# Kernel tuning notes

Hardware: AMD Instinct MI355X
Metric: run time of the kernel (lower is better)

The kernel has to match this reference:

```python
import jax, jax.numpy as jnp
import numpy as np


def setup_inputs() -> dict:
    B, n, C = 256, 512, 256
    key = jax.random.key(0)
    ks = jax.random.split(key, 8)
    s = 1.0 / np.sqrt(C)
    return {
        "P": jax.random.normal(ks[0], (B, n, C), dtype=jnp.float32),
        "id": jax.random.randint(ks[1], (B,), 0, n, dtype=jnp.int64),
        "Wq": jax.random.normal(ks[2], (C, C), dtype=jnp.float32) * s,
        "bq": jax.random.normal(ks[3], (C,), dtype=jnp.float32) * s,
        "Wk": jax.random.normal(ks[4], (C, C), dtype=jnp.float32) * s,
        "bk": jax.random.normal(ks[5], (C,), dtype=jnp.float32) * s,
        "Wv": jax.random.normal(ks[6], (C, C), dtype=jnp.float32) * s,
        "bv": jax.random.normal(ks[7], (C,), dtype=jnp.float32) * s,
    }


def reference(P, id, Wq, bq, Wk, bk, Wv, bv):
    # Gather the query row per batch first, then project (same math as
    # projecting all rows and gathering, but avoids redundant compute).
    B = P.shape[0]
    p_sel = P[jnp.arange(B), id]                 # [B, C]
    Q = p_sel @ Wq.T + bq                        # [B, C]
    K = jnp.einsum('bnc,dc->bnd', P, Wk) + bk    # [B, n, C]
    V = jnp.einsum('bnc,dc->bnd', P, Wv) + bv    # [B, n, C]
    scores = jnp.einsum('bc,bnc->bn', Q, K)      # [B, n] (no sqrt scaling, per source)
    attn = jax.nn.softmax(scores, axis=-1)       # [B, n]
    out = jnp.einsum('bn,bnc->bc', attn, V)      # [B, C]
    return out
```

## Files before the change

kernel.cpp:

```cpp
#include <hip/hip_runtime.h>

#define BATCH 256
#define NROW  512
#define CDIM  256
#define WAVES 8
#define RPW   (NROW / WAVES)
#define CHK   16
#define NCHK  (RPW / CHK)

__global__ __launch_bounds__(256) void qk_kernel(
    const float* __restrict__ P, const int* __restrict__ idx,
    const float* __restrict__ Wq, const float* __restrict__ bq,
    const float* __restrict__ Wk, float* __restrict__ qk) {
  __shared__ float s_psel[CDIM];
  __shared__ float s_q[CDIM];
  const int b = blockIdx.x;
  const int t = threadIdx.x;

  const float* prow = P + ((size_t)b * NROW + (size_t)idx[b]) * CDIM;
  s_psel[t] = prow[t];
  __syncthreads();

  {
    const float4* wq4 = (const float4*)(Wq + (size_t)t * CDIM);
    const float4* ps4 = (const float4*)s_psel;
    float acc = 0.f;
#pragma unroll 8
    for (int c4 = 0; c4 < CDIM / 4; ++c4) {
      float4 w = wq4[c4], p = ps4[c4];
      acc += w.x * p.x + w.y * p.y + w.z * p.z + w.w * p.w;
    }
    s_q[t] = acc + bq[t];
  }
  __syncthreads();

  {
    float acc = 0.f;
#pragma unroll 8
    for (int d = 0; d < CDIM; ++d) acc += s_q[d] * Wk[(size_t)d * CDIM + t];
    qk[(size_t)b * CDIM + t] = acc;
  }
}

__global__ __launch_bounds__(512) void attn_fused_kernel(
    const float* __restrict__ P, const float* __restrict__ qk,
    const float* __restrict__ Wv, const float* __restrict__ bv,
    float* __restrict__ out) {
  const int b = blockIdx.x;
  const int t = threadIdx.x;
  const int lane = t & 63;
  const int w = t >> 6;

  __shared__ float s_ctx[WAVES][CDIM];
  __shared__ float s_m[WAVES], s_l[WAVES];
  __shared__ float s_ctxn[CDIM];
  __shared__ float s_part[2][CDIM];

  const float4 qk4 = ((const float4*)(qk + (size_t)b * CDIM))[lane];
  const float* Pw = P + ((size_t)b * NROW + (size_t)w * RPW) * CDIM;

  float m = -1e30f, l = 0.f;
  float4 ctx = make_float4(0.f, 0.f, 0.f, 0.f);

  for (int ch = 0; ch < NCHK; ++ch) {
    float4 pv[CHK];
#pragma unroll
    for (int i = 0; i < CHK; ++i)
      pv[i] = ((const float4*)(Pw + (size_t)(ch * CHK + i) * CDIM))[lane];

    float sc[CHK];
#pragma unroll
    for (int i = 0; i < CHK; ++i) {
      float part = pv[i].x * qk4.x + pv[i].y * qk4.y +
                   pv[i].z * qk4.z + pv[i].w * qk4.w;
#pragma unroll
      for (int mm = 32; mm >= 1; mm >>= 1) part += __shfl_xor(part, mm, 64);
      sc[i] = part;
    }

    float cmax = sc[0];
#pragma unroll
    for (int i = 1; i < CHK; ++i) cmax = fmaxf(cmax, sc[i]);
    const float mnew = fmaxf(m, cmax);
    const float scale = __expf(m - mnew);
    l *= scale;
    ctx.x *= scale; ctx.y *= scale; ctx.z *= scale; ctx.w *= scale;
#pragma unroll
    for (int i = 0; i < CHK; ++i) {
      const float p = __expf(sc[i] - mnew);
      l += p;
      ctx.x += p * pv[i].x; ctx.y += p * pv[i].y;
      ctx.z += p * pv[i].z; ctx.w += p * pv[i].w;
    }
    m = mnew;
  }

  ((float4*)s_ctx[w])[lane] = ctx;
  if (lane == 0) { s_m[w] = m; s_l[w] = l; }
  __syncthreads();

  if (t < CDIM) {
    float mg = s_m[0];
#pragma unroll
    for (int i = 1; i < WAVES; ++i) mg = fmaxf(mg, s_m[i]);
    float lg = 0.f, c = 0.f;
#pragma unroll
    for (int i = 0; i < WAVES; ++i) {
      const float co = __expf(s_m[i] - mg);
      lg += co * s_l[i];
      c  += co * s_ctx[i][t];
    }
    s_ctxn[t] = c / lg;
  }
  __syncthreads();

  {
    const int d = t & (CDIM - 1);
    const int h = t >> 8;
    const float4* wv4 =
        (const float4*)(Wv + (size_t)d * CDIM + (size_t)h * (CDIM / 2));
    const float4* cx4 = (const float4*)(s_ctxn + h * (CDIM / 2));
    float acc = 0.f;
#pragma unroll 8
    for (int j = 0; j < CDIM / 8; ++j) {
      float4 wv = wv4[j], cc = cx4[j];
      acc += wv.x * cc.x + wv.y * cc.y + wv.z * cc.z + wv.w * cc.w;
    }
    s_part[h][d] = acc;
  }
  __syncthreads();
  if (t < CDIM)
    out[(size_t)b * CDIM + t] = s_part[0][t] + s_part[1][t] + bv[t];
}

extern "C" void kernel_launch(void* const* d_in, const int* in_sizes, int n_in,
                              void* d_out, int out_size, void* d_ws,
                              size_t ws_size, hipStream_t stream) {
  const float* P  = (const float*)d_in[0];
  const int*  idx = (const int*)d_in[1];
  const float* Wq = (const float*)d_in[2];
  const float* bq = (const float*)d_in[3];
  const float* Wk = (const float*)d_in[4];
  const float* Wv = (const float*)d_in[6];
  const float* bv = (const float*)d_in[7];
  float* out = (float*)d_out;

  float* qk = (float*)d_ws;

  qk_kernel<<<BATCH, 256, 0, stream>>>(P, idx, Wq, bq, Wk, qk);
  attn_fused_kernel<<<BATCH, 512, 0, stream>>>(P, qk, Wv, bv, out);
}
```

Measured before the change: 237.7 us.

## Fuse qk projection into attention kernel with double-buffered P prefetch

Merges the separate qk projection kernel into the attention kernel, so there is one launch and qk stays in shared memory instead of going through a global workspace. The first chunk of P rows is loaded before the projection runs, which hides the projection latency behind that load. The row loop is double-buffered with two register buffers of half the old chunk size, prefetching the next chunk while the current one is consumed. In exchange, every block now does the serial projection work inline, with half its threads idle during it, and register pressure grows from holding two buffers.

New measurement: 234.3 us. No clear change (-1.4%).

```diff
diff --git a/kernel.cpp b/kernel.cpp
--- a/kernel.cpp
+++ b/kernel.cpp
@@ -5,95 +5,105 @@
 #define CDIM  256
 #define WAVES 8
 #define RPW   (NROW / WAVES)
-#define CHK   16
+#define CHK   8
 #define NCHK  (RPW / CHK)
 
-__global__ __launch_bounds__(256) void qk_kernel(
+__global__ __launch_bounds__(512) void attn_one_kernel(
     const float* __restrict__ P, const int* __restrict__ idx,
     const float* __restrict__ Wq, const float* __restrict__ bq,
-    const float* __restrict__ Wk, float* __restrict__ qk) {
+    const float* __restrict__ Wk, const float* __restrict__ Wv,
+    const float* __restrict__ bv, float* __restrict__ out) {
+  const int b = blockIdx.x;
+  const int t = threadIdx.x;
+  const int lane = t & 63;
+  const int w = t >> 6;
+
   __shared__ float s_psel[CDIM];
   __shared__ float s_q[CDIM];
-  const int b = blockIdx.x;
-  const int t = threadIdx.x;
+  __shared__ float s_qk[CDIM];
+  __shared__ float s_ctx[WAVES][CDIM];
+  __shared__ float s_m[WAVES], s_l[WAVES];
+  __shared__ float s_ctxn[CDIM];
+  __shared__ float s_part[2][CDIM];
 
-  const float* prow = P + ((size_t)b * NROW + (size_t)idx[b]) * CDIM;
-  s_psel[t] = prow[t];
+  const float* Pw = P + ((size_t)b * NROW + (size_t)w * RPW) * CDIM;
+
+  float4 pv0[CHK], pv1[CHK];
+#pragma unroll
+  for (int i = 0; i < CHK; ++i)
+    pv0[i] = ((const float4*)(Pw + (size_t)i * CDIM))[lane];
+
+  if (t < CDIM)
+    s_psel[t] = P[((size_t)b * NROW + (size_t)idx[b]) * CDIM + t];
   __syncthreads();
 
-  {
+  if (t < CDIM) {
     const float4* wq4 = (const float4*)(Wq + (size_t)t * CDIM);
     const float4* ps4 = (const float4*)s_psel;
     float acc = 0.f;
 #pragma unroll 8
     for (int c4 = 0; c4 < CDIM / 4; ++c4) {
-      float4 w = wq4[c4], p = ps4[c4];
-      acc += w.x * p.x + w.y * p.y + w.z * p.z + w.w * p.w;
+      float4 wv = wq4[c4], p = ps4[c4];
+      acc += wv.x * p.x + wv.y * p.y + wv.z * p.z + wv.w * p.w;
     }
     s_q[t] = acc + bq[t];
   }
   __syncthreads();
 
-  {
+  if (t < CDIM) {
     float acc = 0.f;
 #pragma unroll 8
     for (int d = 0; d < CDIM; ++d) acc += s_q[d] * Wk[(size_t)d * CDIM + t];
-    qk[(size_t)b * CDIM + t] = acc;
+    s_qk[t] = acc;
   }
-}
+  __syncthreads();
 
-__global__ __launch_bounds__(512) void attn_fused_kernel(
-    const float* __restrict__ P, const float* __restrict__ qk,
-    const float* __restrict__ Wv, const float* __restrict__ bv,
-    float* __restrict__ out) {
-  const int b = blockIdx.x;
-  const int t = threadIdx.x;
-  const int lane = t & 63;
-  const int w = t >> 6;
-
-  __shared__ float s_ctx[WAVES][CDIM];
-  __shared__ float s_m[WAVES], s_l[WAVES];
-  __shared__ float s_ctxn[CDIM];
-  __shared__ float s_part[2][CDIM];
-
-  const float4 qk4 = ((const float4*)(qk + (size_t)b * CDIM))[lane];
-  const float* Pw = P + ((size_t)b * NROW + (size_t)w * RPW) * CDIM;
+  const float4 qk4 = ((const float4*)s_qk)[lane];
 
   float m = -1e30f, l = 0.f;
   float4 ctx = make_float4(0.f, 0.f, 0.f, 0.f);
 
-  for (int ch = 0; ch < NCHK; ++ch) {
-    float4 pv[CHK];
+#define PREFETCH(dst, chn)                                                   \
+  {                                                                          \
+    _Pragma("unroll") for (int i = 0; i < CHK; ++i) dst[i] =                 \
+        ((const float4*)(Pw + (size_t)((chn)*CHK + i) * CDIM))[lane];        \
+  }
+
+#define CONSUME(cur)                                                         \
+  {                                                                          \
+    float sc[CHK];                                                           \
+    _Pragma("unroll") for (int i = 0; i < CHK; ++i) {                        \
+      float part = cur[i].x * qk4.x + cur[i].y * qk4.y +                     \
+                   cur[i].z * qk4.z + cur[i].w * qk4.w;                      \
+      _Pragma("unroll") for (int mm = 32; mm >= 1; mm >>= 1)                 \
+          part += __shfl_xor(part, mm, 64);                                  \
+      sc[i] = part;                                                          \
+    }                                                                        \
+    float cmax = sc[0];                                                      \
+    _Pragma("unroll") for (int i = 1; i < CHK; ++i)                          \
+        cmax = fmaxf(cmax, sc[i]);                                           \
+    const float mnew = fmaxf(m, cmax);                                       \
+    const float scale = __expf(m - mnew);       \
+    l *= scale;                                                              \
+    ctx.x *= scale; ctx.y *= scale; ctx.z *= scale; ctx.w *= scale;          \
+    _Pragma("unroll") for (int i = 0; i < CHK; ++i) {                        \
+      const float p = __expf(sc[i] - mnew);                                  \
+      l += p;                                                                \
+      ctx.x += p * cur[i].x; ctx.y += p * cur[i].y;                          \
+      ctx.z += p * cur[i].z; ctx.w += p * cur[i].w;                          \
+    }                                                                        \
+    m = mnew;                                                                \
+  }
+
 #pragma unroll
-    for (int i = 0; i < CHK; ++i)
-      pv[i] = ((const float4*)(Pw + (size_t)(ch * CHK + i) * CDIM))[lane];
-
-    float sc[CHK];
-#pragma unroll
-    for (int i = 0; i < CHK; ++i) {
-      float part = pv[i].x * qk4.x + pv[i].y * qk4.y +
-                   pv[i].z * qk4.z + pv[i].w * qk4.w;
-#pragma unroll
-      for (int mm = 32; mm >= 1; mm >>= 1) part += __shfl_xor(part, mm, 64);
-      sc[i] = part;
-    }
-
-    float cmax = sc[0];
-#pragma unroll
-    for (int i = 1; i < CHK; ++i) cmax = fmaxf(cmax, sc[i]);
-    const float mnew = fmaxf(m, cmax);
-    const float scale = __expf(m - mnew);
-    l *= scale;
-    ctx.x *= scale; ctx.y *= scale; ctx.z *= scale; ctx.w *= scale;
-#pragma unroll
-    for (int i = 0; i < CHK; ++i) {
-      const float p = __expf(sc[i] - mnew);
-      l += p;
-      ctx.x += p * pv[i].x; ctx.y += p * pv[i].y;
-      ctx.z += p * pv[i].z; ctx.w += p * pv[i].w;
-    }
-    m = mnew;
+  for (int cc = 0; cc < NCHK; cc += 2) {
+    if (cc + 1 < NCHK) PREFETCH(pv1, cc + 1);
+    CONSUME(pv0);
+    if (cc + 2 < NCHK) PREFETCH(pv0, cc + 2);
+    if (cc + 1 < NCHK) CONSUME(pv1);
   }
+#undef PREFETCH
+#undef CONSUME
 
   ((float4*)s_ctx[w])[lane] = ctx;
   if (lane == 0) { s_m[w] = m; s_l[w] = l; }
@@ -145,8 +155,5 @@
   const float* bv = (const float*)d_in[7];
   float* out = (float*)d_out;
 
-  float* qk = (float*)d_ws;
-
-  qk_kernel<<<BATCH, 256, 0, stream>>>(P, idx, Wq, bq, Wk, qk);
-  attn_fused_kernel<<<BATCH, 512, 0, stream>>>(P, qk, Wv, bv, out);
+  attn_one_kernel<<<BATCH, 512, 0, stream>>>(P, idx, Wq, bq, Wk, Wv, bv, out);
 }
```
